# Performance work log

Measured on AMD Instinct MI355X. Metric: run time of the kernel, lower is better.

The kernel has to match this reference:

```python
import jax, jax.numpy as jnp
import numpy as np

NUM_HEADS = 16


def _local_attn(q, k, v, bias, nq, nk):
    """Blocked local attention, faithful to rearrange_to_dense_trunk semantics.
    q,k,v: [B,H,N,D]; bias: [B,Hb,N,N] (Hb broadcasts against H).
    Trunk i (queries [i*nq,(i+1)*nq)) attends keys at original indices
    [i*nq - pad_left, i*nq - pad_left + nk); out-of-range keys/values/bias are
    zero-padded (the module pads with zeros, no -inf key masking).
    Assumes N % nq == 0 (q_pad_length == 0, so the query mask loop is a no-op).
    """
    B, H, N, D = q.shape
    T = N // nq                      # n_trunks
    pad_left = (nk - nq) // 2
    Lp = (T - 1) * nq + nk           # padded key length so every window is full
    pad_right = Lp - pad_left - N
    k_p = jnp.pad(k, ((0, 0), (0, 0), (pad_left, pad_right), (0, 0)))
    v_p = jnp.pad(v, ((0, 0), (0, 0), (pad_left, pad_right), (0, 0)))
    b_p = jnp.pad(bias, ((0, 0), (0, 0), (0, 0), (pad_left, pad_right)))
    # window gather indices: [T, nk]
    kidx = jnp.arange(T)[:, None] * nq + jnp.arange(nk)[None, :]
    k_t = k_p[:, :, kidx, :]         # [B,H,T,nk,D]
    v_t = v_p[:, :, kidx, :]         # [B,H,T,nk,D]
    Bb, Hb = bias.shape[0], bias.shape[1]
    b_r = b_p.reshape(Bb, Hb, T, nq, Lp)
    b_t = jnp.take_along_axis(b_r, kidx[None, None, :, None, :], axis=-1)  # [Bb,Hb,T,nq,nk]
    q_t = q.reshape(B, H, T, nq, D)
    scores = jnp.einsum('bhtqd,bhtkd->bhtqk', q_t, k_t) + b_t
    w = jax.nn.softmax(scores, axis=-1)
    o = jnp.einsum('bhtqk,bhtkd->bhtqd', w, v_t)
    return o.reshape(B, H, N, D)


def setup_inputs() -> dict:
    key = jax.random.key(0)
    ks = jax.random.split(key, 8)
    B, N, C = 1, 4096, 256
    H, D = NUM_HEADS, 64
    HD = H * D
    q_x = jax.random.normal(ks[0], (B, N, C), dtype=jnp.float32)
    kv_x = jax.random.normal(ks[1], (B, N, C), dtype=jnp.float32)
    attn_bias = jax.random.normal(ks[2], (B, 1, N, N), dtype=jnp.float32) * 0.1
    Wq = jax.random.normal(ks[3], (C, HD), dtype=jnp.float32) / np.sqrt(C).astype(np.float32)
    Wk = jax.random.normal(ks[4], (C, HD), dtype=jnp.float32) / np.sqrt(C).astype(np.float32)
    Wv = jax.random.normal(ks[5], (C, HD), dtype=jnp.float32) / np.sqrt(C).astype(np.float32)
    Wg = jax.random.normal(ks[6], (C, HD), dtype=jnp.float32) / np.sqrt(C).astype(np.float32)
    Wo = jax.random.normal(ks[7], (HD, C), dtype=jnp.float32) / np.sqrt(HD).astype(np.float32)
    return {"q_x": q_x, "kv_x": kv_x, "attn_bias": attn_bias,
            "Wq": Wq, "Wk": Wk, "Wv": Wv, "Wg": Wg, "Wo": Wo,
            "n_queries": 64, "n_keys": 256}


def reference(q_x, kv_x, attn_bias, Wq, Wk, Wv, Wg, Wo, n_queries, n_keys):
    B, N, C = q_x.shape
    H = NUM_HEADS
    D = Wq.shape[-1] // H
    def split_heads(x):
        return x.reshape(B, N, H, D).transpose(0, 2, 1, 3)  # [B,H,N,D]
    q = split_heads(q_x @ Wq) / jnp.sqrt(jnp.float32(D))
    k = split_heads(kv_x @ Wk)
    v = split_heads(kv_x @ Wv)
    o = _local_attn(q, k, v, attn_bias, n_queries, n_keys)
    o = o.transpose(0, 2, 1, 3).reshape(B, N, H * D)
    g = jax.nn.sigmoid(q_x @ Wg)  # gating head
    return (o * g) @ Wo
```

## Files before the change

### kernel.cpp

```cpp
#include <hip/hip_runtime.h>

#define N_ 4096
#define C_ 256
#define H_ 16
#define D_ 64
#define HD_ 1024

typedef __attribute__((ext_vector_type(8))) _Float16 f16x8;
typedef __attribute__((ext_vector_type(4))) _Float16 f16x4;
typedef __attribute__((ext_vector_type(4))) float f32x4;

__device__ __forceinline__ void gload16(const void* g, void* l) {
    __builtin_amdgcn_global_load_lds(
        (const __attribute__((address_space(1))) unsigned int*)g,
        (__attribute__((address_space(3))) unsigned int*)l, 16, 0, 0);
}

__global__ __launch_bounds__(256) void convert_kernel(
    const float* __restrict__ q_x, const float* __restrict__ kv_x,
    const float* __restrict__ bias,
    const float* __restrict__ Wq, const float* __restrict__ Wk,
    const float* __restrict__ Wv, const float* __restrict__ Wg,
    const float* __restrict__ Wo,
    _Float16* __restrict__ Xf, _Float16* __restrict__ WTf,
    _Float16* __restrict__ WoTf, float* __restrict__ bpF)
{
    __shared__ float ts[64][65];
    const int b = blockIdx.x;
    const int tid = threadIdx.x;

    if (b < 512) {
        const int seg = b >> 8;
        const float* src = seg ? kv_x : q_x;
        _Float16* df = Xf + (size_t)seg * 1048576;
        const int base = (b & 255) * 4096 + tid * 16;
#pragma unroll
        for (int q = 0; q < 4; ++q) {
            float4 v = *(const float4*)&src[base + q * 4];
            f16x4 fv;
            fv[0] = (_Float16)v.x; fv[1] = (_Float16)v.y;
            fv[2] = (_Float16)v.z; fv[3] = (_Float16)v.w;
            *(f16x4*)&df[base + q * 4] = fv;
        }
        return;
    }

    if (b >= 832) {
        const int t = b - 832;
        const int kb = t * 64 - 96;
        float* bpT = bpF + (size_t)t * 16384;
#pragma unroll
        for (int cc = 0; cc < 4; ++cc) {
            if (cc) __syncthreads();
            {
                const int q = tid >> 2;
                const float* brow = bias + (size_t)(t * 64 + q) * 4096;
#pragma unroll
                for (int u = 0; u < 4; ++u) {
                    const int lc = (tid & 3) * 16 + u * 4;
                    const int kg = kb + cc * 64 + lc;
                    float4 v = make_float4(0.f, 0.f, 0.f, 0.f);
                    if ((unsigned)kg < 4093u) v = *(const float4*)&brow[kg];
                    ts[q][lc + 0] = v.x; ts[q][lc + 1] = v.y;
                    ts[q][lc + 2] = v.z; ts[q][lc + 3] = v.w;
                }
            }
            __syncthreads();
            {
                const int s = tid >> 2;
                const int qseg = (tid & 3) * 16;
                float* drow = bpT + (size_t)(cc * 64 + s) * 64 + qseg;
#pragma unroll
                for (int u = 0; u < 4; ++u) {
                    float4 v;
                    v.x = ts[qseg + u * 4 + 0][s];
                    v.y = ts[qseg + u * 4 + 1][s];
                    v.z = ts[qseg + u * 4 + 2][s];
                    v.w = ts[qseg + u * 4 + 3][s];
                    *(float4*)&drow[u * 4] = v;
                }
            }
        }
        return;
    }

    const float* src;
    _Float16* df;
    int srcC, dstC, r0, c0;
    if (b < 768) {
        const int widx = (b - 512) >> 6;
        const int tile = (b - 512) & 63;
        src = (widx == 0) ? Wq : (widx == 1) ? Wk : (widx == 2) ? Wv : Wg;
        df = WTf + (size_t)widx * 262144;
        srcC = 1024; dstC = 256;
        r0 = (tile >> 4) * 64;
        c0 = (tile & 15) * 64;
    } else {
        const int tile = b - 768;
        src = Wo; df = WoTf;
        srcC = 256; dstC = 1024;
        r0 = (tile >> 2) * 64;
        c0 = (tile & 3) * 64;
    }
    {
        const int r = tid >> 2;
        const int cch = (tid & 3) * 16;
#pragma unroll
        for (int q = 0; q < 4; ++q) {
            float4 v = *(const float4*)&src[(size_t)(r0 + r) * srcC + c0 + cch + q * 4];
            ts[r][cch + q * 4 + 0] = v.x;
            ts[r][cch + q * 4 + 1] = v.y;
            ts[r][cch + q * 4 + 2] = v.z;
            ts[r][cch + q * 4 + 3] = v.w;
        }
    }
    __syncthreads();
    {
        const int c = tid >> 2;
        const int rch = (tid & 3) * 16;
#pragma unroll
        for (int q = 0; q < 4; ++q) {
            f16x4 fv;
#pragma unroll
            for (int j = 0; j < 4; ++j)
                fv[j] = (_Float16)ts[rch + q * 4 + j][c];
            *(f16x4*)&df[(size_t)(c0 + c) * dstC + r0 + rch + q * 4] = fv;
        }
    }
}

__global__ __launch_bounds__(256) void proj_mfma(
    const _Float16* __restrict__ Xf, const _Float16* __restrict__ WTf,
    _Float16* __restrict__ qh, _Float16* __restrict__ kh,
    _Float16* __restrict__ vt, _Float16* __restrict__ gh)
{
    __shared__ __align__(16) char psmem[24576];
    _Float16* As = (_Float16*)psmem;
    _Float16* Bs = (_Float16*)(psmem + 8192);

    const int lb  = blockIdx.x;
    const int xcd = lb & 7;
    const int gr  = (lb >> 6) * 8 + xcd;
    const int g   = gr >> 6;
    const int m0  = (gr & 63) * 64;
    const int c0  = ((lb >> 3) & 7) * 128;

    const _Float16* A = Xf + ((g == 1 || g == 2) ? 1048576 : 0);
    const _Float16* B = WTf + (size_t)g * 262144;

    const int tid  = threadIdx.x;
    const int wv   = tid >> 6;
    const int lane = tid & 63;
    const int frow = lane & 15;
    const int grp  = lane >> 4;

    f32x4 acc[8];
#pragma unroll
    for (int j = 0; j < 8; ++j) acc[j] = (f32x4){0.f, 0.f, 0.f, 0.f};

    const int srow = tid >> 3;
    const int sch  = tid & 7;

    for (int kt = 0; kt < 256; kt += 64) {
        __syncthreads();
#pragma unroll
        for (int p = 0; p < 2; ++p) {
            const int row = p * 32 + srow;
            const int koff = kt + ((sch ^ (row & 7)) << 3);
            gload16(A + (size_t)(m0 + row) * 256 + koff, (char*)As + p * 4096 + tid * 16);
        }
#pragma unroll
        for (int p = 0; p < 4; ++p) {
            const int row = p * 32 + srow;
            const int koff = kt + ((sch ^ (row & 7)) << 3);
            gload16(B + (size_t)(c0 + row) * 256 + koff, (char*)Bs + p * 4096 + tid * 16);
        }
        __syncthreads();

#pragma unroll
        for (int ks = 0; ks < 2; ++ks) {
            const int ra = wv * 16 + frow;
            const f16x8 af = *(const f16x8*)((char*)As + ra * 128 + (((ks * 4 + grp) ^ (ra & 7)) << 4));
#pragma unroll
            for (int j = 0; j < 8; ++j) {
                const int rb = j * 16 + frow;
                const f16x8 bf = *(const f16x8*)((char*)Bs + rb * 128 + (((ks * 4 + grp) ^ (rb & 7)) << 4));
                acc[j] = __builtin_amdgcn_mfma_f32_16x16x32_f16(af, bf, acc[j], 0, 0, 0);
            }
        }
    }

    if (g == 2) {
#pragma unroll
        for (int j = 0; j < 8; ++j) {
            const int dglob = c0 + j * 16 + frow;
            const int n = m0 + wv * 16 + grp * 4;
            f16x4 pv;
#pragma unroll
            for (int v = 0; v < 4; ++v) pv[v] = (_Float16)acc[j][v];
            *(f16x4*)&vt[((size_t)dglob << 12) + n] = pv;
        }
        return;
    }

    __syncthreads();
    _Float16* Epi = (_Float16*)psmem;
    {
        const float scale = (g == 0) ? 0.125f : 1.f;
#pragma unroll
        for (int j = 0; j < 8; ++j) {
            const int rr = wv * 16 + grp * 4;
            const int cc = j * 16 + frow;
#pragma unroll
            for (int v = 0; v < 4; ++v) {
                float x = acc[j][v];
                x = (g == 3) ? 1.f / (1.f + __expf(-x)) : x * scale;
                Epi[(rr + v) * 136 + cc] = (_Float16)x;
            }
        }
    }
    __syncthreads();
    {
        const int ch   = tid & 15;
        const int head = ch >> 3;
        const int e8   = (ch & 7) * 8;
#pragma unroll
        for (int p = 0; p < 4; ++p) {
            const int r = p * 16 + (tid >> 4);
            const f16x8 val = *(const f16x8*)&Epi[r * 136 + head * 64 + e8];
            const int n = m0 + r;
            if (g == 3) {
                *(f16x8*)&gh[(size_t)n * HD_ + c0 + head * 64 + e8] = val;
            } else {
                _Float16* dst = (g == 0) ? qh : kh;
                const int hh = (c0 >> 6) + head;
                *(f16x8*)&dst[((size_t)hh * N_ + n) * D_ + e8] = val;
            }
        }
    }
}

__global__ __launch_bounds__(256, 4) void attn_mfma(
    const _Float16* __restrict__ qh, const _Float16* __restrict__ kh,
    const _Float16* __restrict__ vt, const float* __restrict__ bpF,
    const _Float16* __restrict__ gh, _Float16* __restrict__ of)
{
    __shared__ __align__(16) char smem[40960];
    _Float16* Qs = (_Float16*)smem;
    char* Ks = smem + 8192;
    char* Ps = smem;
    char* Vs = smem + 16384;
    float* Oe = (float*)smem;

    const int lb  = blockIdx.x;
    const int xcd = lb & 7;
    const int j_  = lb >> 3;
    const int h   = j_ >> 3;
    const int t   = xcd * 8 + (j_ & 7);
    const int tid = threadIdx.x;
    const int lane = tid & 63;
    const int wv = tid >> 6;
    const int frow = lane & 15;
    const int grp = lane >> 4;
    const int kbase = t * 64 - 96;

    const char* qbase = (const char*)qh + (size_t)(h * N_ + t * 64) * 128;
    const char* kbase_p = (const char*)kh + (size_t)h * N_ * 128;

#pragma unroll
    for (int q = 0; q < 2; ++q) {
        const int lin = q * 4096 + tid * 16;
        const int row = lin >> 7;
        const int ch = (lin >> 4) & 7;
        gload16(qbase + row * 128 + ((ch ^ (row & 7)) << 4), (char*)Qs + lin);
    }
#pragma unroll
    for (int q = 0; q < 8; ++q) {
        const int lin = q * 4096 + tid * 16;
        const int row = lin >> 7;
        const int ch = (lin >> 4) & 7;
        const int kg = kbase + row;
        if ((unsigned)kg < (unsigned)N_) {
            gload16(kbase_p + (size_t)kg * 128 + ((ch ^ (row & 7)) << 4), Ks + lin);
        } else {
            *(float4*)(Ks + lin) = make_float4(0.f, 0.f, 0.f, 0.f);
        }
    }

    f32x4 sacc[16];
    {
        const float* bpT = bpF + (size_t)t * 16384;
        const int q0 = wv * 16 + grp * 4;
#pragma unroll
        for (int j = 0; j < 16; ++j)
            sacc[j] = *(const f32x4*)&bpT[(j * 16 + frow) * 64 + q0];
    }
    __syncthreads();

    {
        const int rq = wv * 16 + frow;
#pragma unroll
        for (int ks = 0; ks < 2; ++ks) {
            const f16x8 aq = *(const f16x8*)((char*)Qs + rq * 128 + (((ks * 4 + grp) ^ (rq & 7)) << 4));
#pragma unroll
            for (int j = 0; j < 16; ++j) {
                const int rk = j * 16 + frow;
                const f16x8 bk = *(const f16x8*)(Ks + rk * 128 + (((ks * 4 + grp) ^ (rk & 7)) << 4));
                sacc[j] = __builtin_amdgcn_mfma_f32_16x16x32_f16(aq, bk, sacc[j], 0, 0, 0);
            }
        }
    }
    __syncthreads();

    float inv[4];
    f32x4 oacc[4];
#pragma unroll
    for (int jd = 0; jd < 4; ++jd) oacc[jd] = (f32x4){0.f, 0.f, 0.f, 0.f};

#pragma unroll
    for (int c = 0; c < 2; ++c) {
        const int cb = kbase + c * 128;
        const bool bnd = (c == 0) ? (t <= 1) : (t >= 62);
        {
#pragma unroll
            for (int q = 0; q < 4; ++q) {
                const int lin = q * 4096 + tid * 16;
                const int d  = lin >> 8;
                const int cs = (lin >> 4) & 15;
                const int cl = (cs & 8) | ((cs & 7) ^ (d & 7));
                const int kg0 = cb + cl * 8;
                const int kgc = kg0 < 0 ? 0 : (kg0 > N_ - 8 ? N_ - 8 : kg0);
                gload16(vt + (((size_t)(h * 64 + d)) << 12) + kgc, Vs + lin);
            }
        }
        if (c == 0) {
#pragma unroll
            for (int v = 0; v < 4; ++v) {
                float m = sacc[0][v];
#pragma unroll
                for (int f = 1; f < 16; ++f) m = fmaxf(m, sacc[f][v]);
                m = fmaxf(m, __shfl_xor(m, 1));
                m = fmaxf(m, __shfl_xor(m, 2));
                m = fmaxf(m, __shfl_xor(m, 4));
                m = fmaxf(m, __shfl_xor(m, 8));
                float l = 0.f;
#pragma unroll
                for (int f = 0; f < 16; ++f) {
                    float e = __expf(sacc[f][v] - m);
                    sacc[f][v] = e;
                    l += e;
                }
                l += __shfl_xor(l, 1);
                l += __shfl_xor(l, 2);
                l += __shfl_xor(l, 4);
                l += __shfl_xor(l, 8);
                inv[v] = 1.f / l;
            }
        }
        {
#pragma unroll
            for (int j = 0; j < 8; ++j) {
#pragma unroll
                for (int v = 0; v < 4; ++v) {
                    const int r = wv * 16 + grp * 4 + v;
                    const int byt = r * 256 + ((j * 32 + frow * 2) ^ ((r & 7) << 4));
                    *(_Float16*)(Ps + byt) = (_Float16)sacc[c * 8 + j][v];
                }
            }
        }
        __syncthreads();
        if (bnd) {
#pragma unroll
            for (int q = 0; q < 4; ++q) {
                const int lin = q * 4096 + tid * 16;
                const int d  = lin >> 8;
                const int cs = (lin >> 4) & 15;
                const int cl = (cs & 8) | ((cs & 7) ^ (d & 7));
                const int kg0 = cb + cl * 8;
                if ((unsigned)kg0 >= (unsigned)N_)
                    *(float4*)(Vs + lin) = make_float4(0.f, 0.f, 0.f, 0.f);
            }
            __syncthreads();
        }
        const int rp = wv * 16 + frow;
#pragma unroll
        for (int ks = 0; ks < 4; ++ks) {
            const f16x8 ap = *(const f16x8*)(Ps + rp * 256 + (((ks * 4 + grp) ^ (rp & 7)) << 4));
#pragma unroll
            for (int jd = 0; jd < 4; ++jd) {
                const int rd = jd * 16 + frow;
                const f16x8 bv = *(const f16x8*)(Vs + rd * 256 + (((ks * 4 + grp) ^ (rd & 7)) << 4));
                oacc[jd] = __builtin_amdgcn_mfma_f32_16x16x32_f16(ap, bv, oacc[jd], 0, 0, 0);
            }
        }
        __syncthreads();
    }

#pragma unroll
    for (int jd = 0; jd < 4; ++jd) {
        const int dcol = jd * 16 + frow;
#pragma unroll
        for (int v = 0; v < 4; ++v) {
            const int rn = wv * 16 + grp * 4 + v;
            Oe[rn * 68 + dcol] = oacc[jd][v] * inv[v];
        }
    }
    __syncthreads();
    {
        const int r   = tid >> 2;
        const int seg = tid & 3;
        const int n   = t * 64 + r;
        const int cg0 = h * 64 + seg * 16;
        const float* orow = &Oe[r * 68 + seg * 16];
        f32x4 o0 = *(const f32x4*)&orow[0];
        f32x4 o1 = *(const f32x4*)&orow[4];
        f32x4 o2 = *(const f32x4*)&orow[8];
        f32x4 o3 = *(const f32x4*)&orow[12];
        const f16x8 g0 = *(const f16x8*)&gh[(size_t)n * HD_ + cg0];
        const f16x8 g1 = *(const f16x8*)&gh[(size_t)n * HD_ + cg0 + 8];
        f16x8 r0, r1;
#pragma unroll
        for (int e = 0; e < 4; ++e) {
            r0[e]     = (_Float16)(o0[e] * (float)g0[e]);
            r0[4 + e] = (_Float16)(o1[e] * (float)g0[4 + e]);
            r1[e]     = (_Float16)(o2[e] * (float)g1[e]);
            r1[4 + e] = (_Float16)(o3[e] * (float)g1[4 + e]);
        }
        *(f16x8*)&of[(size_t)n * HD_ + cg0]     = r0;
        *(f16x8*)&of[(size_t)n * HD_ + cg0 + 8] = r1;
    }
}

__global__ __launch_bounds__(256) void out_mfma(
    const _Float16* __restrict__ of, const _Float16* __restrict__ WoTf,
    float* __restrict__ out)
{
    __shared__ __align__(16) char smem[16384];

    const int lb  = blockIdx.x;
    const int xcd = lb & 7;
    const int s   = lb >> 3;
    const int rowt = (s >> 3) * 8 + xcd;
    const int m0  = rowt * 32;
    const int c0  = (s & 7) * 32;

    const int tid  = threadIdx.x;
    const int wave = tid >> 6;
    const int lane = tid & 63;
    const int wr   = wave >> 1;
    const int wc   = wave & 1;
    const int frow = lane & 15;
    const int grp  = lane >> 4;

    f32x4 acc = (f32x4){0.f, 0.f, 0.f, 0.f};

    auto STAGE = [&](char* bb, int kt) {
        const int row = tid >> 3;
        const int ch  = tid & 7;
        const int koff = kt + ((ch ^ (row & 7)) << 3);
        gload16(of + (size_t)(m0 + row) * HD_ + koff, bb + tid * 16);
        gload16(WoTf + (size_t)(c0 + row) * HD_ + koff, bb + 4096 + tid * 16);
    };

    STAGE(smem, 0);
    __syncthreads();

    for (int t = 0; t < 16; ++t) {
        char* cur = smem + (t & 1) * 8192;
        if (t < 15) STAGE(smem + ((t + 1) & 1) * 8192, (t + 1) * 64);

        _Float16* As = (_Float16*)cur;
        _Float16* Bs = (_Float16*)(cur + 4096);
#pragma unroll
        for (int ks = 0; ks < 2; ++ks) {
            const int ra = wr * 16 + frow;
            const f16x8 af = *(const f16x8*)((char*)As + ra * 128 + (((ks * 4 + grp) ^ (ra & 7)) << 4));
            const int rb = wc * 16 + frow;
            const f16x8 bf = *(const f16x8*)((char*)Bs + rb * 128 + (((ks * 4 + grp) ^ (rb & 7)) << 4));
            acc = __builtin_amdgcn_mfma_f32_16x16x32_f16(af, bf, acc, 0, 0, 0);
        }
        __syncthreads();
    }

    {
        const int c = c0 + wc * 16 + frow;
        const int rbase = grp * 4;
#pragma unroll
        for (int v = 0; v < 4; ++v) {
            const int n = m0 + wr * 16 + rbase + v;
            out[(size_t)n * C_ + c] = acc[v];
        }
    }
}

extern "C" void kernel_launch(void* const* d_in, const int* in_sizes, int n_in,
                              void* d_out, int out_size, void* d_ws, size_t ws_size,
                              hipStream_t stream)
{
    const float* q_x  = (const float*)d_in[0];
    const float* kv_x = (const float*)d_in[1];
    const float* bias = (const float*)d_in[2];
    const float* Wq   = (const float*)d_in[3];
    const float* Wk   = (const float*)d_in[4];
    const float* Wv   = (const float*)d_in[5];
    const float* Wg   = (const float*)d_in[6];
    const float* Wo   = (const float*)d_in[7];
    float* out = (float*)d_out;

    char* ws = (char*)d_ws;
    const size_t MB = 1048576;
    _Float16* qh   = (_Float16*)(ws);
    _Float16* kh   = (_Float16*)(ws + 8  * MB);
    _Float16* vt   = (_Float16*)(ws + 16 * MB);
    _Float16* gh   = (_Float16*)(ws + 24 * MB);
    _Float16* of   = (_Float16*)(ws + 32 * MB);
    _Float16* Xf   = (_Float16*)(ws + 40 * MB);
    _Float16* WTf  = (_Float16*)(ws + 44 * MB);
    _Float16* WoTf = (_Float16*)(ws + 46 * MB);
    float*    bpF  = (float*)   (ws + 48 * MB);

    convert_kernel<<<896, 256, 0, stream>>>(q_x, kv_x, bias, Wq, Wk, Wv, Wg, Wo,
                                            Xf, WTf, WoTf, bpF);
    proj_mfma<<<2048, 256, 0, stream>>>(Xf, WTf, qh, kh, vt, gh);
    attn_mfma<<<1024, 256, 0, stream>>>(qh, kh, vt, bpF, gh, of);
    out_mfma<<<1024, 256, 0, stream>>>(of, WoTf, out);
}
```

Before: 161.6 us.

## Split attention work across 8 waves with cross-wave softmax reduction

Attention blocks now launch 512 threads. The 256-key window is split between two wave halves for QK^T, and the D dimension is split for PV. Row max and row sum are exchanged between halves through shared memory, and the first V chunk load is issued before the softmax. The aim is to halve per-wave register pressure and raise occupancy and latency hiding, at the cost of extra barriers and LDS exchange traffic.

Measured after the change: 176.7 us. 1.09x slower.

```diff
diff --git a/kernel.cpp b/kernel.cpp
--- a/kernel.cpp
+++ b/kernel.cpp
@@ -240,14 +240,15 @@
     }
 }
 
-__global__ __launch_bounds__(256, 4) void attn_mfma(
+__global__ __launch_bounds__(512, 8) void attn_mfma(
     const _Float16* __restrict__ qh, const _Float16* __restrict__ kh,
     const _Float16* __restrict__ vt, const float* __restrict__ bpF,
     const _Float16* __restrict__ gh, _Float16* __restrict__ of)
 {
     __shared__ __align__(16) char smem[40960];
-    _Float16* Qs = (_Float16*)smem;
-    char* Ks = smem + 8192;
+    char* Ks = smem;
+    _Float16* Qs = (_Float16*)(smem + 32768);
+    float* Xch = (float*)(smem + 32768);
     char* Ps = smem;
     char* Vs = smem + 16384;
     float* Oe = (float*)smem;
@@ -260,6 +261,8 @@
     const int tid = threadIdx.x;
     const int lane = tid & 63;
     const int wv = tid >> 6;
+    const int wq = wv & 3;
+    const int wh = wv >> 2;
     const int frow = lane & 15;
     const int grp = lane >> 4;
     const int kbase = t * 64 - 96;
@@ -267,16 +270,15 @@
     const char* qbase = (const char*)qh + (size_t)(h * N_ + t * 64) * 128;
     const char* kbase_p = (const char*)kh + (size_t)h * N_ * 128;
 
-#pragma unroll
-    for (int q = 0; q < 2; ++q) {
-        const int lin = q * 4096 + tid * 16;
+    {
+        const int lin = tid * 16;
         const int row = lin >> 7;
         const int ch = (lin >> 4) & 7;
         gload16(qbase + row * 128 + ((ch ^ (row & 7)) << 4), (char*)Qs + lin);
     }
 #pragma unroll
-    for (int q = 0; q < 8; ++q) {
-        const int lin = q * 4096 + tid * 16;
+    for (int q = 0; q < 4; ++q) {
+        const int lin = q * 8192 + tid * 16;
         const int row = lin >> 7;
         const int ch = (lin >> 4) & 7;
         const int kg = kbase + row;
@@ -287,24 +289,24 @@
         }
     }
 
-    f32x4 sacc[16];
+    f32x4 sacc[8];
     {
         const float* bpT = bpF + (size_t)t * 16384;
-        const int q0 = wv * 16 + grp * 4;
-#pragma unroll
-        for (int j = 0; j < 16; ++j)
-            sacc[j] = *(const f32x4*)&bpT[(j * 16 + frow) * 64 + q0];
-    }
-    __syncthreads();
-
-    {
-        const int rq = wv * 16 + frow;
+        const int q0 = wq * 16 + grp * 4;
+#pragma unroll
+        for (int j = 0; j < 8; ++j)
+            sacc[j] = *(const f32x4*)&bpT[(wh * 128 + j * 16 + frow) * 64 + q0];
+    }
+    __syncthreads();
+
+    {
+        const int rq = wq * 16 + frow;
 #pragma unroll
         for (int ks = 0; ks < 2; ++ks) {
             const f16x8 aq = *(const f16x8*)((char*)Qs + rq * 128 + (((ks * 4 + grp) ^ (rq & 7)) << 4));
 #pragma unroll
-            for (int j = 0; j < 16; ++j) {
-                const int rk = j * 16 + frow;
+            for (int j = 0; j < 8; ++j) {
+                const int rk = wh * 128 + j * 16 + frow;
                 const f16x8 bk = *(const f16x8*)(Ks + rk * 128 + (((ks * 4 + grp) ^ (rk & 7)) << 4));
                 sacc[j] = __builtin_amdgcn_mfma_f32_16x16x32_f16(aq, bk, sacc[j], 0, 0, 0);
             }
@@ -312,19 +314,83 @@
     }
     __syncthreads();
 
-    float inv[4];
-    f32x4 oacc[4];
-#pragma unroll
-    for (int jd = 0; jd < 4; ++jd) oacc[jd] = (f32x4){0.f, 0.f, 0.f, 0.f};
+    {
+        const int cb = kbase;
+#pragma unroll
+        for (int q = 0; q < 2; ++q) {
+            const int lin = q * 8192 + tid * 16;
+            const int d  = lin >> 8;
+            const int cs = (lin >> 4) & 15;
+            const int cl = (cs & 8) | ((cs & 7) ^ (d & 7));
+            const int kg0 = cb + cl * 8;
+            const int kgc = kg0 < 0 ? 0 : (kg0 > N_ - 8 ? N_ - 8 : kg0);
+            gload16(vt + (((size_t)(h * 64 + d)) << 12) + kgc, Vs + lin);
+        }
+    }
+
+    float mp[4], inv[4];
+#pragma unroll
+    for (int v = 0; v < 4; ++v) {
+        float m = sacc[0][v];
+#pragma unroll
+        for (int f = 1; f < 8; ++f) m = fmaxf(m, sacc[f][v]);
+        m = fmaxf(m, __shfl_xor(m, 1));
+        m = fmaxf(m, __shfl_xor(m, 2));
+        m = fmaxf(m, __shfl_xor(m, 4));
+        m = fmaxf(m, __shfl_xor(m, 8));
+        mp[v] = m;
+    }
+    if (frow == 0) {
+#pragma unroll
+        for (int v = 0; v < 4; ++v)
+            Xch[wh * 64 + wq * 16 + grp * 4 + v] = mp[v];
+    }
+    __syncthreads();
+    {
+        float lp[4];
+#pragma unroll
+        for (int v = 0; v < 4; ++v) {
+            const float mo = Xch[(1 - wh) * 64 + wq * 16 + grp * 4 + v];
+            const float m = fmaxf(mp[v], mo);
+            mp[v] = m;
+            float l = 0.f;
+#pragma unroll
+            for (int f = 0; f < 8; ++f) {
+                float e = __expf(sacc[f][v] - m);
+                sacc[f][v] = e;
+                l += e;
+            }
+            l += __shfl_xor(l, 1);
+            l += __shfl_xor(l, 2);
+            l += __shfl_xor(l, 4);
+            l += __shfl_xor(l, 8);
+            lp[v] = l;
+        }
+        if (frow == 0) {
+#pragma unroll
+            for (int v = 0; v < 4; ++v)
+                Xch[128 + wh * 64 + wq * 16 + grp * 4 + v] = lp[v];
+        }
+        __syncthreads();
+#pragma unroll
+        for (int v = 0; v < 4; ++v) {
+            const float lo = Xch[128 + (1 - wh) * 64 + wq * 16 + grp * 4 + v];
+            inv[v] = 1.f / (lp[v] + lo);
+        }
+    }
+
+    f32x4 oacc[2];
+#pragma unroll
+    for (int jd = 0; jd < 2; ++jd) oacc[jd] = (f32x4){0.f, 0.f, 0.f, 0.f};
 
 #pragma unroll
     for (int c = 0; c < 2; ++c) {
         const int cb = kbase + c * 128;
         const bool bnd = (c == 0) ? (t <= 1) : (t >= 62);
-        {
-#pragma unroll
-            for (int q = 0; q < 4; ++q) {
-                const int lin = q * 4096 + tid * 16;
+        if (c == 1) {
+#pragma unroll
+            for (int q = 0; q < 2; ++q) {
+                const int lin = q * 8192 + tid * 16;
                 const int d  = lin >> 8;
                 const int cs = (lin >> 4) & 15;
                 const int cl = (cs & 8) | ((cs & 7) ^ (d & 7));
@@ -333,46 +399,22 @@
                 gload16(vt + (((size_t)(h * 64 + d)) << 12) + kgc, Vs + lin);
             }
         }
-        if (c == 0) {
-#pragma unroll
-            for (int v = 0; v < 4; ++v) {
-                float m = sacc[0][v];
-#pragma unroll
-                for (int f = 1; f < 16; ++f) m = fmaxf(m, sacc[f][v]);
-                m = fmaxf(m, __shfl_xor(m, 1));
-                m = fmaxf(m, __shfl_xor(m, 2));
-                m = fmaxf(m, __shfl_xor(m, 4));
-                m = fmaxf(m, __shfl_xor(m, 8));
-                float l = 0.f;
-#pragma unroll
-                for (int f = 0; f < 16; ++f) {
-                    float e = __expf(sacc[f][v] - m);
-                    sacc[f][v] = e;
-                    l += e;
-                }
-                l += __shfl_xor(l, 1);
-                l += __shfl_xor(l, 2);
-                l += __shfl_xor(l, 4);
-                l += __shfl_xor(l, 8);
-                inv[v] = 1.f / l;
-            }
-        }
-        {
+        if (wh == c) {
 #pragma unroll
             for (int j = 0; j < 8; ++j) {
 #pragma unroll
                 for (int v = 0; v < 4; ++v) {
-                    const int r = wv * 16 + grp * 4 + v;
+                    const int r = wq * 16 + grp * 4 + v;
                     const int byt = r * 256 + ((j * 32 + frow * 2) ^ ((r & 7) << 4));
-                    *(_Float16*)(Ps + byt) = (_Float16)sacc[c * 8 + j][v];
+                    *(_Float16*)(Ps + byt) = (_Float16)sacc[j][v];
                 }
             }
         }
         __syncthreads();
         if (bnd) {
 #pragma unroll
-            for (int q = 0; q < 4; ++q) {
-                const int lin = q * 4096 + tid * 16;
+            for (int q = 0; q < 2; ++q) {
+                const int lin = q * 8192 + tid * 16;
                 const int d  = lin >> 8;
                 const int cs = (lin >> 4) & 15;
                 const int cl = (cs & 8) | ((cs & 7) ^ (d & 7));
@@ -382,52 +424,48 @@
             }
             __syncthreads();
         }
-        const int rp = wv * 16 + frow;
-#pragma unroll
-        for (int ks = 0; ks < 4; ++ks) {
-            const f16x8 ap = *(const f16x8*)(Ps + rp * 256 + (((ks * 4 + grp) ^ (rp & 7)) << 4));
-#pragma unroll
-            for (int jd = 0; jd < 4; ++jd) {
-                const int rd = jd * 16 + frow;
-                const f16x8 bv = *(const f16x8*)(Vs + rd * 256 + (((ks * 4 + grp) ^ (rd & 7)) << 4));
-                oacc[jd] = __builtin_amdgcn_mfma_f32_16x16x32_f16(ap, bv, oacc[jd], 0, 0, 0);
+        {
+            const int rp = wq * 16 + frow;
+#pragma unroll
+            for (int ks = 0; ks < 4; ++ks) {
+                const f16x8 ap = *(const f16x8*)(Ps + rp * 256 + (((ks * 4 + grp) ^ (rp & 7)) << 4));
+#pragma unroll
+                for (int jd = 0; jd < 2; ++jd) {
+                    const int rd = wh * 32 + jd * 16 + frow;
+                    const f16x8 bv = *(const f16x8*)(Vs + rd * 256 + (((ks * 4 + grp) ^ (rd & 7)) << 4));
+                    oacc[jd] = __builtin_amdgcn_mfma_f32_16x16x32_f16(ap, bv, oacc[jd], 0, 0, 0);
+                }
             }
         }
         __syncthreads();
     }
 
 #pragma unroll
-    for (int jd = 0; jd < 4; ++jd) {
-        const int dcol = jd * 16 + frow;
+    for (int jd = 0; jd < 2; ++jd) {
+        const int dcol = wh * 32 + jd * 16 + frow;
 #pragma unroll
         for (int v = 0; v < 4; ++v) {
-            const int rn = wv * 16 + grp * 4 + v;
+            const int rn = wq * 16 + grp * 4 + v;
             Oe[rn * 68 + dcol] = oacc[jd][v] * inv[v];
         }
     }
     __syncthreads();
     {
-        const int r   = tid >> 2;
-        const int seg = tid & 3;
+        const int r   = tid >> 3;
+        const int seg = tid & 7;
         const int n   = t * 64 + r;
-        const int cg0 = h * 64 + seg * 16;
-        const float* orow = &Oe[r * 68 + seg * 16];
+        const int cg0 = h * 64 + seg * 8;
+        const float* orow = &Oe[r * 68 + seg * 8];
         f32x4 o0 = *(const f32x4*)&orow[0];
         f32x4 o1 = *(const f32x4*)&orow[4];
-        f32x4 o2 = *(const f32x4*)&orow[8];
-        f32x4 o3 = *(const f32x4*)&orow[12];
         const f16x8 g0 = *(const f16x8*)&gh[(size_t)n * HD_ + cg0];
-        const f16x8 g1 = *(const f16x8*)&gh[(size_t)n * HD_ + cg0 + 8];
-        f16x8 r0, r1;
+        f16x8 r0;
 #pragma unroll
         for (int e = 0; e < 4; ++e) {
             r0[e]     = (_Float16)(o0[e] * (float)g0[e]);
             r0[4 + e] = (_Float16)(o1[e] * (float)g0[4 + e]);
-            r1[e]     = (_Float16)(o2[e] * (float)g1[e]);
-            r1[4 + e] = (_Float16)(o3[e] * (float)g1[4 + e]);
-        }
-        *(f16x8*)&of[(size_t)n * HD_ + cg0]     = r0;
-        *(f16x8*)&of[(size_t)n * HD_ + cg0 + 8] = r1;
+        }
+        *(f16x8*)&of[(size_t)n * HD_ + cg0] = r0;
     }
 }
 
@@ -522,6 +560,6 @@
     convert_kernel<<<896, 256, 0, stream>>>(q_x, kv_x, bias, Wq, Wk, Wv, Wg, Wo,
                                             Xf, WTf, WoTf, bpF);
     proj_mfma<<<2048, 256, 0, stream>>>(Xf, WTf, qh, kh, vt, gh);
-    attn_mfma<<<1024, 256, 0, stream>>>(qh, kh, vt, bpF, gh, of);
+    attn_mfma<<<1024, 512, 0, stream>>>(qh, kh, vt, bpF, gh, of);
     out_mfma<<<1024, 256, 0, stream>>>(of, WoTf, out);
 }
```
